# Optimization experiments

Measured on AMD Instinct MI355X. Metric: run time of the kernel, lower is better.

The kernel has to match this reference:

```python
import jax, jax.numpy as jnp
import numpy as np

EPS = 1e-6  # AngularPhysicsConfig.eps


def setup_inputs() -> dict:
    key = jax.random.key(0)
    k1, k2 = jax.random.split(key)
    B, L, d, H = 2, 2048, 2048, 8
    x_spatial = jax.random.normal(k1, (B, L, d), dtype=jnp.float32)
    # attn is a softmax output: rows sum to 1 over the last axis
    attn = jax.nn.softmax(jax.random.normal(k2, (B, H, L, L), dtype=jnp.float32), axis=-1)
    W = jnp.ones((1,), dtype=jnp.float32)   # nn.Parameter(torch.ones(1))
    b = jnp.zeros((1,), dtype=jnp.float32)  # bias_init = 0.0
    return {"x_spatial": x_spatial, "attn": attn, "W": W, "b": b}


def reference(x_spatial, attn, W, b):
    # --- angular_kernel ---
    norm = jnp.clip(jnp.linalg.norm(x_spatial, axis=-1, keepdims=True), EPS, None)
    x_unit = x_spatial / norm                                   # [B, L, d]
    K = jnp.einsum('bld,bmd->blm', x_unit, x_unit)              # [B, L, L] cosine sim
    K_mean = K.mean(axis=(-1, -2), keepdims=True)
    K_cent = K - K_mean
    # torch .std() is unbiased (ddof=1), computed on detached K_cent
    K_std = jnp.std(jax.lax.stop_gradient(K_cent), axis=(-1, -2), keepdims=True, ddof=1)
    K_norm = K_cent / jnp.clip(K_std, EPS, None)                # [B, L, L]

    # --- compute_cos_align (detach_attn_for_alignment=True) ---
    A = jax.lax.stop_gradient(attn.mean(axis=1))                # [B, L, L]
    cos_align = jnp.sum(A * K_norm, axis=-1)                    # [B, L]

    # --- gate ---
    gate = jax.nn.sigmoid(W * cos_align + b)                    # [B, L]
    return gate, cos_align, K_norm
```

## Files before the change

### kernel.cpp

```cpp
#include <hip/hip_runtime.h>
#include <hip/hip_bf16.h>

#define L_DIM 2048
#define D_DIM 2048
#define B_DIM 2
#define H_DIM 8
#define NT 16
#define NPAIR 136
#define NRED 512
#define NKT (D_DIM / 32)
#define EPSV 1e-6f

using bf16x8 = __attribute__((ext_vector_type(8))) __bf16;
using f32x4  = __attribute__((ext_vector_type(4))) float;
using f4     = __attribute__((ext_vector_type(4))) float;
using us4    = __attribute__((ext_vector_type(4))) unsigned short;

__device__ inline void gload_lds16(const void* g, void* l) {
    __builtin_amdgcn_global_load_lds(
        (const __attribute__((address_space(1))) void*)g,
        (__attribute__((address_space(3))) void*)l, 16, 0, 0);
}

__device__ inline ushort f2bf(float f) {
    unsigned int u = __float_as_uint(f);
    unsigned int lsb = (u >> 16) & 1u;
    u += 0x7fffu + lsb;
    return (ushort)(u >> 16);
}
__device__ inline float bf2f(ushort u) {
    return __uint_as_float(((unsigned int)u) << 16);
}

__global__ __launch_bounds__(256) void k_normalize(const float* __restrict__ x,
                                                   ushort* __restrict__ xu,
                                                   double* __restrict__ sums) {
    const int row = blockIdx.x;
    const int t   = threadIdx.x;
    const float* xr = x + (size_t)row * D_DIM;
    f4 v0 = __builtin_nontemporal_load(((const f4*)xr) + t);
    f4 v1 = __builtin_nontemporal_load(((const f4*)xr) + t + 256);
    float ss = v0.x*v0.x + v0.y*v0.y + v0.z*v0.z + v0.w*v0.w
             + v1.x*v1.x + v1.y*v1.y + v1.z*v1.z + v1.w*v1.w;
    #pragma unroll
    for (int off = 32; off; off >>= 1) ss += __shfl_down(ss, off);
    __shared__ float red[4];
    __shared__ float s_inv;
    if ((t & 63) == 0) red[t >> 6] = ss;
    __syncthreads();
    if (t == 0) {
        float nrm = sqrtf(red[0] + red[1] + red[2] + red[3]);
        nrm = fmaxf(nrm, EPSV);
        s_inv = 1.0f / nrm;
        if (row == 0) { sums[0] = 0.0; sums[1] = 0.0; sums[2] = 0.0; sums[3] = 0.0; }
    }
    __syncthreads();
    const float inv = s_inv;
    ushort* xo = xu + (size_t)row * D_DIM;
    ushort4 o0, o1;
    o0.x = f2bf(v0.x * inv); o0.y = f2bf(v0.y * inv);
    o0.z = f2bf(v0.z * inv); o0.w = f2bf(v0.w * inv);
    o1.x = f2bf(v1.x * inv); o1.y = f2bf(v1.y * inv);
    o1.z = f2bf(v1.z * inv); o1.w = f2bf(v1.w * inv);
    ((ushort4*)xo)[t]       = o0;
    ((ushort4*)xo)[t + 256] = o1;
}

__global__ __launch_bounds__(256) void k_mixed(const ushort* __restrict__ Xu,
                                               const float* __restrict__ attn,
                                               float* __restrict__ Kout,
                                               double* __restrict__ sums,
                                               ushort* __restrict__ Amean) {
    __shared__ __align__(16) ushort lds_a[2][128 * 32];
    __shared__ __align__(16) ushort lds_b[2][128 * 32];
    const int t = threadIdx.x;
    const int batch = blockIdx.z;

    if (blockIdx.x >= NPAIR) {
        const int rid = blockIdx.x - NPAIR;
        const float* ab = attn + (size_t)batch * H_DIM * L_DIM * L_DIM;
        ushort* am = Amean + (size_t)batch * L_DIM * L_DIM;
        const int n4 = L_DIM * L_DIM / 4;
        for (int i = rid * 256 + t; i < n4; i += NRED * 256) {
            float4 s = {0.f, 0.f, 0.f, 0.f};
            #pragma unroll
            for (int h = 0; h < H_DIM; ++h) {
                const f4 v = __builtin_nontemporal_load(
                    ((const f4*)(ab + (size_t)h * L_DIM * L_DIM)) + i);
                s.x += v.x; s.y += v.y; s.z += v.z; s.w += v.w;
            }
            ushort4 o;
            o.x = f2bf(s.x * 0.125f); o.y = f2bf(s.y * 0.125f);
            o.z = f2bf(s.z * 0.125f); o.w = f2bf(s.w * 0.125f);
            ((ushort4*)am)[i] = o;
        }
        return;
    }

    const int lane = t & 63;
    const int w    = t >> 6;
    const int wr   = w >> 1, wc = w & 1;
    int ti = 0, rem = blockIdx.x;
    while (rem >= NT - ti) { rem -= NT - ti; ++ti; }
    const int tj = ti + rem;
    const int bRow = ti * 128;
    const int bCol = tj * 128;
    const bool diag = (ti == tj);
    const ushort* Xb = Xu + (size_t)batch * L_DIM * D_DIM;

    const int srow = t >> 2;
    const int scol = ((t & 3) ^ ((srow >> 1) & 3)) * 8;
    const ushort* gA0 = Xb + (size_t)(bRow + srow)      * D_DIM + scol;
    const ushort* gA1 = Xb + (size_t)(bRow + 64 + srow) * D_DIM + scol;
    const ushort* gB0 = Xb + (size_t)(bCol + srow)      * D_DIM + scol;
    const ushort* gB1 = Xb + (size_t)(bCol + 64 + srow) * D_DIM + scol;
    const int ldst = t * 8;

    f32x4 acc[4][4] = {};
    const int frow = lane & 15;
    const int fk   = lane >> 4;
    const int fx   = (frow >> 1) & 3;

    auto STAGE = [&](int buf, int kt) {
        const size_t ko = (size_t)kt * 32;
        gload_lds16(gA0 + ko, &lds_a[buf][ldst]);
        gload_lds16(gA1 + ko, &lds_a[buf][64 * 32 + ldst]);
        gload_lds16(gB0 + ko, &lds_b[buf][ldst]);
        gload_lds16(gB1 + ko, &lds_b[buf][64 * 32 + ldst]);
    };
    auto COMPUTE = [&](int buf) {
        bf16x8 a[4], b[4];
        #pragma unroll
        for (int m = 0; m < 4; ++m)
            a[m] = *(const bf16x8*)&lds_a[buf][(wr * 64 + m * 16 + frow) * 32 + (fk ^ fx) * 8];
        #pragma unroll
        for (int n = 0; n < 4; ++n)
            b[n] = *(const bf16x8*)&lds_b[buf][(wc * 64 + n * 16 + frow) * 32 + (fk ^ fx) * 8];
        #pragma unroll
        for (int m = 0; m < 4; ++m)
            #pragma unroll
            for (int n = 0; n < 4; ++n)
                acc[m][n] = __builtin_amdgcn_mfma_f32_16x16x32_bf16(a[m], b[n], acc[m][n], 0, 0, 0);
    };

    STAGE(0, 0);
    __syncthreads();
    for (int kt = 0; kt < NKT; kt += 2) {
        STAGE(1, kt + 1);
        COMPUTE(0);
        __syncthreads();
        if (kt + 2 < NKT) STAGE(0, kt + 2);
        COMPUTE(1);
        __syncthreads();
    }

    float* Kb = Kout + (size_t)batch * L_DIM * L_DIM;
    float ps = 0.f, pss = 0.f;
    #pragma unroll
    for (int m = 0; m < 4; ++m) {
        #pragma unroll
        for (int n = 0; n < 4; ++n) {
            #pragma unroll
            for (int j = 0; j < 4; ++j) {
                const int r = bRow + wr * 64 + m * 16 + fk * 4 + j;
                const int c = bCol + wc * 64 + n * 16 + frow;
                const float v = acc[m][n][j];
                Kb[(size_t)r * L_DIM + c] = v;
                ps += v; pss += v * v;
            }
            if (!diag) {
                const int rr  = bCol + wc * 64 + n * 16 + frow;
                const int cc0 = bRow + wr * 64 + m * 16 + fk * 4;
                *(float4*)&Kb[(size_t)rr * L_DIM + cc0] = *(float4*)&acc[m][n];
            }
        }
    }
    if (!diag) { ps *= 2.f; pss *= 2.f; }
    #pragma unroll
    for (int off = 32; off; off >>= 1) {
        ps  += __shfl_down(ps, off);
        pss += __shfl_down(pss, off);
    }
    __shared__ float redS[4], redSS[4];
    if (lane == 0) { redS[w] = ps; redSS[w] = pss; }
    __syncthreads();
    if (t == 0) {
        atomicAdd(&sums[batch * 2],     (double)(redS[0] + redS[1] + redS[2] + redS[3]));
        atomicAdd(&sums[batch * 2 + 1], (double)(redSS[0] + redSS[1] + redSS[2] + redSS[3]));
    }
}

__global__ __launch_bounds__(256) void k_epilogue(float* __restrict__ out,
                                                  const ushort* __restrict__ Amean,
                                                  const double* __restrict__ sums,
                                                  const float* __restrict__ Wp,
                                                  const float* __restrict__ bp) {
    const int row = blockIdx.x;
    const int b = row >> 11;
    const int t = threadIdx.x;

    const double N = (double)L_DIM * (double)L_DIM;
    const double mean_d = sums[b * 2] / N;
    double var = (sums[b * 2 + 1] - N * mean_d * mean_d) / (N - 1.0);
    var = var > 0.0 ? var : 0.0;
    float sd = (float)sqrt(var);
    sd = fmaxf(sd, EPSV);
    const float inv_std = 1.0f / sd;
    const float mean = (float)mean_d;

    float* Krow = out + 2 * B_DIM * L_DIM + (size_t)row * L_DIM;
    const ushort* arow = Amean + (size_t)row * L_DIM;

    f4 k0 = ((const f4*)Krow)[t * 2];
    f4 k1 = ((const f4*)Krow)[t * 2 + 1];
    const ushort4 a0 = ((const ushort4*)arow)[t * 2];
    const ushort4 a1 = ((const ushort4*)arow)[t * 2 + 1];
    float dot = bf2f(a0.x) * k0.x + bf2f(a0.y) * k0.y + bf2f(a0.z) * k0.z + bf2f(a0.w) * k0.w
              + bf2f(a1.x) * k1.x + bf2f(a1.y) * k1.y + bf2f(a1.z) * k1.z + bf2f(a1.w) * k1.w;
    f4 n0, n1;
    n0.x = (k0.x - mean) * inv_std; n0.y = (k0.y - mean) * inv_std;
    n0.z = (k0.z - mean) * inv_std; n0.w = (k0.w - mean) * inv_std;
    n1.x = (k1.x - mean) * inv_std; n1.y = (k1.y - mean) * inv_std;
    n1.z = (k1.z - mean) * inv_std; n1.w = (k1.w - mean) * inv_std;
    __builtin_nontemporal_store(n0, ((f4*)Krow) + t * 2);
    __builtin_nontemporal_store(n1, ((f4*)Krow) + t * 2 + 1);

    #pragma unroll
    for (int off = 32; off; off >>= 1) dot += __shfl_down(dot, off);
    __shared__ float red[4];
    if ((t & 63) == 0) red[t >> 6] = dot;
    __syncthreads();
    if (t == 0) {
        const float dotv = red[0] + red[1] + red[2] + red[3];
        const float ca = (dotv - mean) * inv_std;
        out[B_DIM * L_DIM + row] = ca;
        const float z = Wp[0] * ca + bp[0];
        out[row] = 1.0f / (1.0f + expf(-z));
    }
}

extern "C" void kernel_launch(void* const* d_in, const int* in_sizes, int n_in,
                              void* d_out, int out_size, void* d_ws, size_t ws_size,
                              hipStream_t stream) {
    const float* x    = (const float*)d_in[0];
    const float* attn = (const float*)d_in[1];
    const float* W    = (const float*)d_in[2];
    const float* bb   = (const float*)d_in[3];
    float* out = (float*)d_out;

    const size_t XU_BYTES = (size_t)B_DIM * L_DIM * D_DIM * 2;
    ushort* xu    = (ushort*)d_ws;
    double* sums  = (double*)((char*)d_ws + XU_BYTES);
    ushort* Amean = (ushort*)((char*)d_ws + XU_BYTES + 256);
    float*  Kbuf  = out + 2 * B_DIM * L_DIM;

    hipLaunchKernelGGL(k_normalize, dim3(B_DIM * L_DIM), dim3(256), 0, stream,
                       x, xu, sums);
    hipLaunchKernelGGL(k_mixed, dim3(NPAIR + NRED, 1, B_DIM), dim3(256), 0, stream,
                       xu, attn, Kbuf, sums, Amean);
    hipLaunchKernelGGL(k_epilogue, dim3(B_DIM * L_DIM), dim3(256), 0, stream,
                       out, Amean, sums, W, bb);
}
```

Before: 109.5 us.

## Store raw K in bf16 workspace and move part of attn reduction into prep kernel

The raw cosine-similarity matrix is written as bf16 into workspace instead of fp32 into the output, halving the intermediate write and epilogue read. A quarter of the attention head-mean reduction is moved into the normalization kernel so it runs alongside the row normalization. The normalized output and cos_align now derive from bf16-rounded K values, which reduces precision.

New measurement: 113.3 us. 1.03x slower.

```diff
diff --git a/kernel.cpp b/kernel.cpp
--- a/kernel.cpp
+++ b/kernel.cpp
@@ -8,13 +8,14 @@
 #define NT 16
 #define NPAIR 136
 #define NRED 512
+#define NRED_A 128
+#define NRED_B (NRED - NRED_A)
 #define NKT (D_DIM / 32)
 #define EPSV 1e-6f
 
 using bf16x8 = __attribute__((ext_vector_type(8))) __bf16;
 using f32x4  = __attribute__((ext_vector_type(4))) float;
 using f4     = __attribute__((ext_vector_type(4))) float;
-using us4    = __attribute__((ext_vector_type(4))) unsigned short;
 
 __device__ inline void gload_lds16(const void* g, void* l) {
     __builtin_amdgcn_global_load_lds(
@@ -32,11 +33,39 @@
     return __uint_as_float(((unsigned int)u) << 16);
 }
 
-__global__ __launch_bounds__(256) void k_normalize(const float* __restrict__ x,
-                                                   ushort* __restrict__ xu,
-                                                   double* __restrict__ sums) {
-    const int row = blockIdx.x;
-    const int t   = threadIdx.x;
+__device__ inline void reduce_chunk(const float* __restrict__ attn, ushort* __restrict__ Amean,
+                                    int batch, int rid, int t) {
+    const float* ab = attn + (size_t)batch * H_DIM * L_DIM * L_DIM;
+    ushort* am = Amean + (size_t)batch * L_DIM * L_DIM;
+    int i = rid * 256 + t;
+    #pragma unroll
+    for (int j = 0; j < 8; ++j, i += NRED * 256) {
+        float4 s = {0.f, 0.f, 0.f, 0.f};
+        #pragma unroll
+        for (int h = 0; h < H_DIM; ++h) {
+            const f4 v = __builtin_nontemporal_load(
+                ((const f4*)(ab + (size_t)h * L_DIM * L_DIM)) + i);
+            s.x += v.x; s.y += v.y; s.z += v.z; s.w += v.w;
+        }
+        ushort4 o;
+        o.x = f2bf(s.x * 0.125f); o.y = f2bf(s.y * 0.125f);
+        o.z = f2bf(s.z * 0.125f); o.w = f2bf(s.w * 0.125f);
+        ((ushort4*)am)[i] = o;
+    }
+}
+
+__global__ __launch_bounds__(256) void k_prep(const float* __restrict__ x,
+                                              const float* __restrict__ attn,
+                                              ushort* __restrict__ xu,
+                                              double* __restrict__ sums,
+                                              ushort* __restrict__ Amean) {
+    const int t = threadIdx.x;
+    const int bid = blockIdx.x;
+    if (bid < 2 * NRED_A) {
+        reduce_chunk(attn, Amean, bid >> 7, bid & (NRED_A - 1), t);
+        return;
+    }
+    const int row = bid - 2 * NRED_A;
     const float* xr = x + (size_t)row * D_DIM;
     f4 v0 = __builtin_nontemporal_load(((const f4*)xr) + t);
     f4 v1 = __builtin_nontemporal_load(((const f4*)xr) + t + 256);
@@ -68,7 +97,7 @@
 
 __global__ __launch_bounds__(256) void k_mixed(const ushort* __restrict__ Xu,
                                                const float* __restrict__ attn,
-                                               float* __restrict__ Kout,
+                                               ushort* __restrict__ K16,
                                                double* __restrict__ sums,
                                                ushort* __restrict__ Amean) {
     __shared__ __align__(16) ushort lds_a[2][128 * 32];
@@ -77,23 +106,7 @@
     const int batch = blockIdx.z;
 
     if (blockIdx.x >= NPAIR) {
-        const int rid = blockIdx.x - NPAIR;
-        const float* ab = attn + (size_t)batch * H_DIM * L_DIM * L_DIM;
-        ushort* am = Amean + (size_t)batch * L_DIM * L_DIM;
-        const int n4 = L_DIM * L_DIM / 4;
-        for (int i = rid * 256 + t; i < n4; i += NRED * 256) {
-            float4 s = {0.f, 0.f, 0.f, 0.f};
-            #pragma unroll
-            for (int h = 0; h < H_DIM; ++h) {
-                const f4 v = __builtin_nontemporal_load(
-                    ((const f4*)(ab + (size_t)h * L_DIM * L_DIM)) + i);
-                s.x += v.x; s.y += v.y; s.z += v.z; s.w += v.w;
-            }
-            ushort4 o;
-            o.x = f2bf(s.x * 0.125f); o.y = f2bf(s.y * 0.125f);
-            o.z = f2bf(s.z * 0.125f); o.w = f2bf(s.w * 0.125f);
-            ((ushort4*)am)[i] = o;
-        }
+        reduce_chunk(attn, Amean, batch, NRED_A + (blockIdx.x - NPAIR), t);
         return;
     }
 
@@ -154,7 +167,7 @@
         __syncthreads();
     }
 
-    float* Kb = Kout + (size_t)batch * L_DIM * L_DIM;
+    ushort* Kb = K16 + (size_t)batch * L_DIM * L_DIM;
     float ps = 0.f, pss = 0.f;
     #pragma unroll
     for (int m = 0; m < 4; ++m) {
@@ -165,13 +178,16 @@
                 const int r = bRow + wr * 64 + m * 16 + fk * 4 + j;
                 const int c = bCol + wc * 64 + n * 16 + frow;
                 const float v = acc[m][n][j];
-                Kb[(size_t)r * L_DIM + c] = v;
+                Kb[(size_t)r * L_DIM + c] = f2bf(v);
                 ps += v; pss += v * v;
             }
             if (!diag) {
                 const int rr  = bCol + wc * 64 + n * 16 + frow;
                 const int cc0 = bRow + wr * 64 + m * 16 + fk * 4;
-                *(float4*)&Kb[(size_t)rr * L_DIM + cc0] = *(float4*)&acc[m][n];
+                ushort4 mq;
+                mq.x = f2bf(acc[m][n][0]); mq.y = f2bf(acc[m][n][1]);
+                mq.z = f2bf(acc[m][n][2]); mq.w = f2bf(acc[m][n][3]);
+                *(ushort4*)&Kb[(size_t)rr * L_DIM + cc0] = mq;
             }
         }
     }
@@ -191,6 +207,7 @@
 }
 
 __global__ __launch_bounds__(256) void k_epilogue(float* __restrict__ out,
+                                                  const ushort* __restrict__ K16,
                                                   const ushort* __restrict__ Amean,
                                                   const double* __restrict__ sums,
                                                   const float* __restrict__ Wp,
@@ -208,22 +225,28 @@
     const float inv_std = 1.0f / sd;
     const float mean = (float)mean_d;
 
-    float* Krow = out + 2 * B_DIM * L_DIM + (size_t)row * L_DIM;
+    const ushort* krow = K16 + (size_t)row * L_DIM;
     const ushort* arow = Amean + (size_t)row * L_DIM;
-
-    f4 k0 = ((const f4*)Krow)[t * 2];
-    f4 k1 = ((const f4*)Krow)[t * 2 + 1];
+    float* onrm = out + 2 * B_DIM * L_DIM + (size_t)row * L_DIM;
+
+    const ushort4 k0 = ((const ushort4*)krow)[t * 2];
+    const ushort4 k1 = ((const ushort4*)krow)[t * 2 + 1];
     const ushort4 a0 = ((const ushort4*)arow)[t * 2];
     const ushort4 a1 = ((const ushort4*)arow)[t * 2 + 1];
-    float dot = bf2f(a0.x) * k0.x + bf2f(a0.y) * k0.y + bf2f(a0.z) * k0.z + bf2f(a0.w) * k0.w
-              + bf2f(a1.x) * k1.x + bf2f(a1.y) * k1.y + bf2f(a1.z) * k1.z + bf2f(a1.w) * k1.w;
+    float kf[8] = { bf2f(k0.x), bf2f(k0.y), bf2f(k0.z), bf2f(k0.w),
+                    bf2f(k1.x), bf2f(k1.y), bf2f(k1.z), bf2f(k1.w) };
+    float af[8] = { bf2f(a0.x), bf2f(a0.y), bf2f(a0.z), bf2f(a0.w),
+                    bf2f(a1.x), bf2f(a1.y), bf2f(a1.z), bf2f(a1.w) };
+    float dot = 0.f;
+    #pragma unroll
+    for (int j = 0; j < 8; ++j) dot += af[j] * kf[j];
     f4 n0, n1;
-    n0.x = (k0.x - mean) * inv_std; n0.y = (k0.y - mean) * inv_std;
-    n0.z = (k0.z - mean) * inv_std; n0.w = (k0.w - mean) * inv_std;
-    n1.x = (k1.x - mean) * inv_std; n1.y = (k1.y - mean) * inv_std;
-    n1.z = (k1.z - mean) * inv_std; n1.w = (k1.w - mean) * inv_std;
-    __builtin_nontemporal_store(n0, ((f4*)Krow) + t * 2);
-    __builtin_nontemporal_store(n1, ((f4*)Krow) + t * 2 + 1);
+    n0.x = (kf[0] - mean) * inv_std; n0.y = (kf[1] - mean) * inv_std;
+    n0.z = (kf[2] - mean) * inv_std; n0.w = (kf[3] - mean) * inv_std;
+    n1.x = (kf[4] - mean) * inv_std; n1.y = (kf[5] - mean) * inv_std;
+    n1.z = (kf[6] - mean) * inv_std; n1.w = (kf[7] - mean) * inv_std;
+    __builtin_nontemporal_store(n0, ((f4*)onrm) + t * 2);
+    __builtin_nontemporal_store(n1, ((f4*)onrm) + t * 2 + 1);
 
     #pragma unroll
     for (int off = 32; off; off >>= 1) dot += __shfl_down(dot, off);
@@ -248,16 +271,16 @@
     const float* bb   = (const float*)d_in[3];
     float* out = (float*)d_out;
 
-    const size_t XU_BYTES = (size_t)B_DIM * L_DIM * D_DIM * 2;
+    const size_t MAT = (size_t)B_DIM * L_DIM * L_DIM;
     ushort* xu    = (ushort*)d_ws;
-    double* sums  = (double*)((char*)d_ws + XU_BYTES);
-    ushort* Amean = (ushort*)((char*)d_ws + XU_BYTES + 256);
-    float*  Kbuf  = out + 2 * B_DIM * L_DIM;
-
-    hipLaunchKernelGGL(k_normalize, dim3(B_DIM * L_DIM), dim3(256), 0, stream,
-                       x, xu, sums);
-    hipLaunchKernelGGL(k_mixed, dim3(NPAIR + NRED, 1, B_DIM), dim3(256), 0, stream,
-                       xu, attn, Kbuf, sums, Amean);
+    double* sums  = (double*)((char*)d_ws + MAT * 2);
+    ushort* Amean = (ushort*)((char*)d_ws + MAT * 2 + 256);
+    ushort* K16   = (ushort*)((char*)d_ws + MAT * 4 + 256);
+
+    hipLaunchKernelGGL(k_prep, dim3(2 * NRED_A + B_DIM * L_DIM), dim3(256), 0, stream,
+                       x, attn, xu, sums, Amean);
+    hipLaunchKernelGGL(k_mixed, dim3(NPAIR + NRED_B, 1, B_DIM), dim3(256), 0, stream,
+                       xu, attn, K16, sums, Amean);
     hipLaunchKernelGGL(k_epilogue, dim3(B_DIM * L_DIM), dim3(256), 0, stream,
-                       out, Amean, sums, W, bb);
-}
+                       out, K16, Amean, sums, W, bb);
+}
```
